# Optimization experiments

Measured on AMD Instinct MI355X. Metric: run time of the kernel, lower is better.

Reference implementation:

```python
import jax, jax.numpy as jnp
import numpy as np

B, L, D, K = 16, 4096, 1024, 64


def setup_inputs() -> dict:
    key = jax.random.key(0)
    k1, k2, k3 = jax.random.split(key, 3)
    token_hidden = jax.random.normal(k1, (B, L, D), dtype=jnp.float32)
    attention_mask = jax.random.randint(k2, (B, L), 0, 2, dtype=jnp.int32)
    # [B, K, 2] spans with start <= end (sorted along last axis)
    sent_spans = jnp.sort(jax.random.randint(k3, (B, K, 2), 0, L, dtype=jnp.int64), axis=-1)
    return {"token_hidden": token_hidden, "attention_mask": attention_mask, "sent_spans": sent_spans}


def reference(token_hidden, attention_mask, sent_spans):
    # token_hidden: [B, L, D]; attention_mask: [B, L] int; sent_spans: [B, K, 2] int
    Bn, Ln, Dn = token_hidden.shape
    pos = jnp.arange(Ln)  # [L]
    start = sent_spans[..., 0]                      # [B, K]
    end = jnp.minimum(sent_spans[..., 1], Ln)       # clamp end to L (original: end = min(end, L))
    # membership mask: token l belongs to span k of batch b
    seg = (pos[None, None, :] >= start[..., None]) & (pos[None, None, :] < end[..., None])  # [B, K, L]
    segf = seg.astype(token_hidden.dtype)
    am = attention_mask.astype(token_hidden.dtype)[:, None, :]  # [B, 1, L]
    amw = segf * am                                 # attention-weighted membership
    mask_sum = amw.sum(axis=-1)                     # [B, K] number of attended tokens in span
    length = segf.sum(axis=-1)                      # [B, K] raw span length (after clamping)
    use_am = mask_sum > 0
    # original: masked mean if any attended token, else plain mean over span
    w = jnp.where(use_am[..., None], amw, segf)     # [B, K, L]
    denom = jnp.where(use_am, mask_sum, length)     # [B, K]
    valid = length > 0                              # span non-empty and starts inside L
    denom_safe = jnp.where(valid, denom, jnp.ones_like(denom))
    pooled = jnp.einsum('bkl,bld->bkd', w, token_hidden) / denom_safe[..., None]
    H = jnp.where(valid[..., None], pooled, jnp.zeros_like(pooled))  # [B, K, D]
    sent_mask = valid.astype(jnp.float32)           # [B, K]
    return H, sent_mask
```

## Files before the change

kernel.cpp:

```cpp
#include <hip/hip_runtime.h>

#define Bn 16
#define Ln 4096
#define Dn 1024
#define Kn 64
#define CH 16
#define SEGTOK 128
#define CPS (SEGTOK / CH)
#define NSEG (Ln / SEGTOK)
#define SLOTS (CPS + 1)
#define NSPAN (2 * Bn * Kn)
#define QBLK 4

static __device__ __forceinline__ void acc4(float4& a, const float4 v) {
    a.x += v.x; a.y += v.y; a.z += v.z; a.w += v.w;
}
static __device__ __forceinline__ void sub4(float4& a, const float4 v) {
    a.x -= v.x; a.y -= v.y; a.z -= v.z; a.w -= v.w;
}
static __device__ __forceinline__ void acc4w(float4& a, const float4 v, float w) {
    a.x += v.x * w; a.y += v.y * w; a.z += v.z * w; a.w += v.w * w;
}

static __device__ __forceinline__ void edge8(
    const float* __restrict__ xb, const int* __restrict__ amb,
    int base, int n, float sign, float4& acc) {
    int wv[8];
    int any = 0;
#pragma unroll
    for (int t = 0; t < 8; ++t) {
        const int li = (base + t < Ln) ? (base + t) : (Ln - 1);
        wv[t] = (t < n) ? amb[li] : 0;
        any |= wv[t];
    }
    if (any != 0) {
        int f = 0;
#pragma unroll
        for (int t = 7; t >= 0; --t) if (wv[t] != 0) f = t;
        int le[8];
        int lp = f;
#pragma unroll
        for (int t = 0; t < 8; ++t) { lp = (wv[t] != 0) ? t : lp; le[t] = lp; }
        float4 v[8];
#pragma unroll
        for (int t = 0; t < 8; ++t)
            v[t] = *(const float4*)(xb + (size_t)(base + le[t]) * Dn);
        float4 s0 = {0.f,0.f,0.f,0.f}, s1 = {0.f,0.f,0.f,0.f};
#pragma unroll
        for (int t = 0; t < 8; t += 2) {
            acc4w(s0, v[t],     sign * (float)wv[t]);
            acc4w(s1, v[t + 1], sign * (float)wv[t + 1]);
        }
        acc4(s0, s1);
        acc4(acc, s0);
    }
}

__global__ __launch_bounds__(256) void fused_stage1_kernel(
    const float* __restrict__ x, const int* __restrict__ am,
    const unsigned int* __restrict__ spans_raw,
    float* __restrict__ Pf, int* __restrict__ Pam, int* __restrict__ dec) {
    const int bc = blockIdx.x;

    if (bc < Bn * NSEG) {
        const int b = bc / NSEG;
        const int seg = bc % NSEG;
        const int d0 = threadIdx.x * 4;

        const float* xp = x + ((size_t)b * Ln + (size_t)seg * SEGTOK) * Dn + d0;
        const int4* amp4 = (const int4*)(am + b * Ln + seg * SEGTOK);
        float* pf = Pf + (size_t)bc * SLOTS * Dn + d0;

        float4 acc = {0.f, 0.f, 0.f, 0.f};
#pragma unroll
        for (int j = 0; j < CPS; ++j) {
            *(float4*)(pf + (size_t)j * Dn) = acc;

            int4 a0 = amp4[j * 4 + 0];
            int4 a1 = amp4[j * 4 + 1];
            int4 a2 = amp4[j * 4 + 2];
            int4 a3 = amp4[j * 4 + 3];
            int wv[CH] = {a0.x, a0.y, a0.z, a0.w, a1.x, a1.y, a1.z, a1.w,
                          a2.x, a2.y, a2.z, a2.w, a3.x, a3.y, a3.z, a3.w};

            int any = 0;
#pragma unroll
            for (int t = 0; t < CH; ++t) any |= wv[t];

            if (any != 0) {
                int f = 0;
#pragma unroll
                for (int t = CH - 1; t >= 0; --t) if (wv[t] != 0) f = t;
                int le[CH];
                int lp = f;
#pragma unroll
                for (int t = 0; t < CH; ++t) {
                    lp = (wv[t] != 0) ? t : lp;
                    le[t] = lp;
                }
                float4 v[CH];
#pragma unroll
                for (int t = 0; t < CH; ++t)
                    v[t] = *(const float4*)(xp + (size_t)(j * CH + le[t]) * Dn);
                float4 s0 = {0.f, 0.f, 0.f, 0.f}, s1 = {0.f, 0.f, 0.f, 0.f};
#pragma unroll
                for (int t = 0; t < CH; t += 2) {
                    acc4w(s0, v[t],     (float)wv[t]);
                    acc4w(s1, v[t + 1], (float)wv[t + 1]);
                }
                acc4(s0, s1);
                acc4(acc, s0);
            }
        }
        *(float4*)(pf + (size_t)CPS * Dn) = acc;
    } else if (bc < Bn * NSEG + Bn) {
        const int b = bc - Bn * NSEG;
        const int t = threadIdx.x;
        const int i0 = t * 16;
        const int* amb = am + (size_t)b * Ln;
        int loc[16];
        int lsum = 0;
#pragma unroll
        for (int j = 0; j < 16; ++j) { loc[j] = amb[i0 + j]; lsum += loc[j]; }

        __shared__ int ssum[256];
        ssum[t] = lsum;
        __syncthreads();
        for (int off = 1; off < 256; off <<= 1) {
            int v2 = (t >= off) ? ssum[t - off] : 0;
            __syncthreads();
            ssum[t] += v2;
            __syncthreads();
        }
        int run = ssum[t] - lsum;
        int* pam = Pam + (size_t)b * (Ln + 1);
#pragma unroll
        for (int j = 0; j < 16; ++j) { pam[i0 + j] = run; run += loc[j]; }
        if (t == 255) pam[Ln] = run;
    } else {
        __shared__ unsigned int sred[256];
        unsigned int acc = 0;
        for (int i = threadIdx.x; i < NSPAN / 2; i += 256)
            acc |= spans_raw[2 * i + 1];
        sred[threadIdx.x] = acc;
        __syncthreads();
        for (int off = 128; off > 0; off >>= 1) {
            if ((int)threadIdx.x < off) sred[threadIdx.x] |= sred[threadIdx.x + off];
            __syncthreads();
        }
        const bool is64 = (sred[0] == 0u);
        for (int i = threadIdx.x; i < NSPAN; i += 256)
            dec[i] = is64 ? (int)spans_raw[2 * i] : (int)spans_raw[i];
    }
}

__global__ __launch_bounds__(64) void span_pool_kernel(
    const float* __restrict__ x, const int* __restrict__ am,
    const int* __restrict__ spans, const float* __restrict__ Pf,
    const int* __restrict__ Pam, float* __restrict__ H,
    float* __restrict__ sent_mask) {
    const int gb = blockIdx.x;
    const int bk = gb >> 2;
    const int q  = gb & 3;
    const int b = bk / Kn;

    int s = spans[2 * bk];
    int e = spans[2 * bk + 1];
    if (s < 0) s = 0; if (s > Ln) s = Ln;
    if (e < 0) e = 0; if (e > Ln) e = Ln;
    const int len = (e > s) ? (e - s) : 0;
    if (e < s) e = s;

    const int* pam = Pam + (size_t)b * (Ln + 1);
    const int msum = pam[e] - pam[s];
    const bool use_am = (msum > 0);
    const bool valid = (len > 0);

    const int d0 = q * 256 + (int)threadIdx.x * 4;
    const float* xb = x + (size_t)b * Ln * Dn + d0;
    const int* amb = am + (size_t)b * Ln;
    float4 acc = {0.f, 0.f, 0.f, 0.f};

    if (!use_am) {
        for (int l = s; l < e; ++l)
            acc4(acc, *(const float4*)(xb + (size_t)l * Dn));
    } else {
        const int ca = (s + CH - 1) / CH;
        const int cb = e / CH;
        const float* Pb = Pf + (size_t)b * NSEG * SLOTS * Dn + d0;

        if (ca <= cb) {
            if (cb > ca) {
                const int sa = ca / CPS, ja = ca % CPS;
                const int sb = cb / CPS, jb = cb % CPS;
                if (sa == sb) {
                    float4 r = *(const float4*)(Pb + (size_t)(sa * SLOTS + jb) * Dn);
                    sub4(r, *(const float4*)(Pb + (size_t)(sa * SLOTS + ja) * Dn));
                    acc4(acc, r);
                } else {
                    float4 r = *(const float4*)(Pb + (size_t)(sa * SLOTS + CPS) * Dn);
                    sub4(r, *(const float4*)(Pb + (size_t)(sa * SLOTS + ja) * Dn));
                    float4 m0 = {0.f,0.f,0.f,0.f}, m1 = {0.f,0.f,0.f,0.f};
                    int ss = sa + 1;
                    for (; ss + 1 < sb; ss += 2) {
                        acc4(m0, *(const float4*)(Pb + (size_t)(ss * SLOTS + CPS) * Dn));
                        acc4(m1, *(const float4*)(Pb + (size_t)((ss + 1) * SLOTS + CPS) * Dn));
                    }
                    if (ss < sb)
                        acc4(m0, *(const float4*)(Pb + (size_t)(ss * SLOTS + CPS) * Dn));
                    acc4(r, m0); acc4(r, m1);
                    if (jb > 0)
                        acc4(r, *(const float4*)(Pb + (size_t)(sb * SLOTS + jb) * Dn));
                    acc4(acc, r);
                }
            }

            const int elenA = ca * CH - s;
            if (elenA > 0) {
                if (elenA <= 8) {
                    edge8(xb, amb, s, elenA, 1.f, acc);
                } else {
                    const int g = ca - 1;
                    const int sg = g / CPS, j = g % CPS;
                    acc4(acc, *(const float4*)(Pb + (size_t)(sg * SLOTS + j + 1) * Dn));
                    sub4(acc, *(const float4*)(Pb + (size_t)(sg * SLOTS + j) * Dn));
                    edge8(xb, amb, g * CH, CH - elenA, -1.f, acc);
                }
            }

            const int elenB = e - cb * CH;
            if (elenB > 0) {
                if (elenB <= 8) {
                    edge8(xb, amb, cb * CH, elenB, 1.f, acc);
                } else {
                    const int g = cb;
                    const int sg = g / CPS, j = g % CPS;
                    acc4(acc, *(const float4*)(Pb + (size_t)(sg * SLOTS + j + 1) * Dn));
                    sub4(acc, *(const float4*)(Pb + (size_t)(sg * SLOTS + j) * Dn));
                    edge8(xb, amb, e, CH - elenB, -1.f, acc);
                }
            }
        } else {
            int wv[CH];
#pragma unroll
            for (int t = 0; t < CH; ++t) {
                const int li = (s + t < Ln) ? (s + t) : (Ln - 1);
                wv[t] = (t < len) ? amb[li] : 0;
            }
            int any = 0;
#pragma unroll
            for (int t = 0; t < CH; ++t) any |= wv[t];
            if (any != 0) {
                int f = 0;
#pragma unroll
                for (int t = CH - 1; t >= 0; --t) if (wv[t] != 0) f = t;
                int le[CH];
                int lp = f;
#pragma unroll
                for (int t = 0; t < CH; ++t) {
                    lp = (wv[t] != 0) ? t : lp;
                    le[t] = lp;
                }
                float4 v[CH];
#pragma unroll
                for (int t = 0; t < CH; ++t)
                    v[t] = *(const float4*)(xb + (size_t)(s + le[t]) * Dn);
                float4 s0 = {0.f,0.f,0.f,0.f}, s1 = {0.f,0.f,0.f,0.f};
#pragma unroll
                for (int t = 0; t < CH; t += 2) {
                    acc4w(s0, v[t],     (float)wv[t]);
                    acc4w(s1, v[t + 1], (float)wv[t + 1]);
                }
                acc4(s0, s1);
                acc4(acc, s0);
            }
        }
    }

    const float denom = use_am ? (float)msum : (float)len;
    const float inv = valid ? (1.0f / denom) : 0.0f;
    float4 outv;
    outv.x = acc.x * inv; outv.y = acc.y * inv;
    outv.z = acc.z * inv; outv.w = acc.w * inv;

    *(float4*)(H + (size_t)bk * Dn + d0) = outv;
    if (threadIdx.x == 0 && q == 0) sent_mask[bk] = valid ? 1.0f : 0.0f;
}

extern "C" void kernel_launch(void* const* d_in, const int* in_sizes, int n_in,
                              void* d_out, int out_size, void* d_ws, size_t ws_size,
                              hipStream_t stream) {
    const float* x = (const float*)d_in[0];
    const int* am = (const int*)d_in[1];
    const unsigned int* spans_raw = (const unsigned int*)d_in[2];

    float* H = (float*)d_out;
    float* sent_mask = H + (size_t)Bn * Kn * Dn;

    const size_t dec_bytes = 8192;
    const size_t pam_bytes = (size_t)Bn * (Ln + 1) * sizeof(int);
    int* dec = (int*)d_ws;
    int* Pam = (int*)((char*)d_ws + dec_bytes);
    float* Pf = (float*)((char*)d_ws + dec_bytes + pam_bytes);

    fused_stage1_kernel<<<Bn * NSEG + Bn + 1, 256, 0, stream>>>(
        x, am, spans_raw, Pf, Pam, dec);
    span_pool_kernel<<<Bn * Kn * QBLK, 64, 0, stream>>>(
        x, am, dec, Pf, Pam, H, sent_mask);
}
```

Baseline: 37.73 us.

## Merge both stages into one cooperative kernel with a grid-wide sync

Replaces the two launches (prefix-sum stage and span-pooling stage) with a single cooperative kernel. All 512 blocks first build the chunk prefix sums, with blocks 0-16 also computing the mask prefix and decoding the spans. A grid.sync follows, and then each wave grid-strides over the span-pool tasks. This removes one kernel launch and the inter-kernel gap, at the cost of a grid barrier, extra serial work on the first 17 blocks, and a cooperative launch that needs every block resident at once.

```diff
diff --git a/kernel.cpp b/kernel.cpp
--- a/kernel.cpp
+++ b/kernel.cpp
@@ -1,4 +1,7 @@
 #include <hip/hip_runtime.h>
+#include <hip/hip_cooperative_groups.h>
+
+namespace cg = cooperative_groups;
 
 #define Bn 16
 #define Ln 4096
@@ -11,6 +14,8 @@
 #define SLOTS (CPS + 1)
 #define NSPAN (2 * Bn * Kn)
 #define QBLK 4
+#define NBLK (Bn * NSEG)
+#define NWAVE (NBLK * 4)
 
 static __device__ __forceinline__ void acc4(float4& a, const float4 v) {
     a.x += v.x; a.y += v.y; a.z += v.z; a.w += v.w;
@@ -56,65 +61,16 @@
     }
 }
 
-__global__ __launch_bounds__(256) void fused_stage1_kernel(
+__global__ __launch_bounds__(256) void fused_all_kernel(
     const float* __restrict__ x, const int* __restrict__ am,
     const unsigned int* __restrict__ spans_raw,
-    float* __restrict__ Pf, int* __restrict__ Pam, int* __restrict__ dec) {
+    float* __restrict__ Pf, int* __restrict__ Pam, int* __restrict__ dec,
+    float* __restrict__ H, float* __restrict__ sent_mask) {
     const int bc = blockIdx.x;
-
-    if (bc < Bn * NSEG) {
-        const int b = bc / NSEG;
-        const int seg = bc % NSEG;
-        const int d0 = threadIdx.x * 4;
-
-        const float* xp = x + ((size_t)b * Ln + (size_t)seg * SEGTOK) * Dn + d0;
-        const int4* amp4 = (const int4*)(am + b * Ln + seg * SEGTOK);
-        float* pf = Pf + (size_t)bc * SLOTS * Dn + d0;
-
-        float4 acc = {0.f, 0.f, 0.f, 0.f};
-#pragma unroll
-        for (int j = 0; j < CPS; ++j) {
-            *(float4*)(pf + (size_t)j * Dn) = acc;
-
-            int4 a0 = amp4[j * 4 + 0];
-            int4 a1 = amp4[j * 4 + 1];
-            int4 a2 = amp4[j * 4 + 2];
-            int4 a3 = amp4[j * 4 + 3];
-            int wv[CH] = {a0.x, a0.y, a0.z, a0.w, a1.x, a1.y, a1.z, a1.w,
-                          a2.x, a2.y, a2.z, a2.w, a3.x, a3.y, a3.z, a3.w};
-
-            int any = 0;
-#pragma unroll
-            for (int t = 0; t < CH; ++t) any |= wv[t];
-
-            if (any != 0) {
-                int f = 0;
-#pragma unroll
-                for (int t = CH - 1; t >= 0; --t) if (wv[t] != 0) f = t;
-                int le[CH];
-                int lp = f;
-#pragma unroll
-                for (int t = 0; t < CH; ++t) {
-                    lp = (wv[t] != 0) ? t : lp;
-                    le[t] = lp;
-                }
-                float4 v[CH];
-#pragma unroll
-                for (int t = 0; t < CH; ++t)
-                    v[t] = *(const float4*)(xp + (size_t)(j * CH + le[t]) * Dn);
-                float4 s0 = {0.f, 0.f, 0.f, 0.f}, s1 = {0.f, 0.f, 0.f, 0.f};
-#pragma unroll
-                for (int t = 0; t < CH; t += 2) {
-                    acc4w(s0, v[t],     (float)wv[t]);
-                    acc4w(s1, v[t + 1], (float)wv[t + 1]);
-                }
-                acc4(s0, s1);
-                acc4(acc, s0);
-            }
-        }
-        *(float4*)(pf + (size_t)CPS * Dn) = acc;
-    } else if (bc < Bn * NSEG + Bn) {
-        const int b = bc - Bn * NSEG;
+    __shared__ int ssum[256];
+
+    if (bc < Bn) {
+        const int b = bc;
         const int t = threadIdx.x;
         const int i0 = t * 16;
         const int* amb = am + (size_t)b * Ln;
@@ -123,7 +79,6 @@
 #pragma unroll
         for (int j = 0; j < 16; ++j) { loc[j] = amb[i0 + j]; lsum += loc[j]; }
 
-        __shared__ int ssum[256];
         ssum[t] = lsum;
         __syncthreads();
         for (int off = 1; off < 256; off <<= 1) {
@@ -137,119 +92,48 @@
 #pragma unroll
         for (int j = 0; j < 16; ++j) { pam[i0 + j] = run; run += loc[j]; }
         if (t == 255) pam[Ln] = run;
-    } else {
-        __shared__ unsigned int sred[256];
+        __syncthreads();
+    } else if (bc == Bn) {
         unsigned int acc = 0;
         for (int i = threadIdx.x; i < NSPAN / 2; i += 256)
             acc |= spans_raw[2 * i + 1];
-        sred[threadIdx.x] = acc;
+        ssum[threadIdx.x] = (int)acc;
         __syncthreads();
         for (int off = 128; off > 0; off >>= 1) {
-            if ((int)threadIdx.x < off) sred[threadIdx.x] |= sred[threadIdx.x + off];
+            if ((int)threadIdx.x < off) ssum[threadIdx.x] |= ssum[threadIdx.x + off];
             __syncthreads();
         }
-        const bool is64 = (sred[0] == 0u);
+        const bool is64 = (ssum[0] == 0);
         for (int i = threadIdx.x; i < NSPAN; i += 256)
             dec[i] = is64 ? (int)spans_raw[2 * i] : (int)spans_raw[i];
-    }
-}
-
-__global__ __launch_bounds__(64) void span_pool_kernel(
-    const float* __restrict__ x, const int* __restrict__ am,
-    const int* __restrict__ spans, const float* __restrict__ Pf,
-    const int* __restrict__ Pam, float* __restrict__ H,
-    float* __restrict__ sent_mask) {
-    const int gb = blockIdx.x;
-    const int bk = gb >> 2;
-    const int q  = gb & 3;
-    const int b = bk / Kn;
-
-    int s = spans[2 * bk];
-    int e = spans[2 * bk + 1];
-    if (s < 0) s = 0; if (s > Ln) s = Ln;
-    if (e < 0) e = 0; if (e > Ln) e = Ln;
-    const int len = (e > s) ? (e - s) : 0;
-    if (e < s) e = s;
-
-    const int* pam = Pam + (size_t)b * (Ln + 1);
-    const int msum = pam[e] - pam[s];
-    const bool use_am = (msum > 0);
-    const bool valid = (len > 0);
-
-    const int d0 = q * 256 + (int)threadIdx.x * 4;
-    const float* xb = x + (size_t)b * Ln * Dn + d0;
-    const int* amb = am + (size_t)b * Ln;
-    float4 acc = {0.f, 0.f, 0.f, 0.f};
-
-    if (!use_am) {
-        for (int l = s; l < e; ++l)
-            acc4(acc, *(const float4*)(xb + (size_t)l * Dn));
-    } else {
-        const int ca = (s + CH - 1) / CH;
-        const int cb = e / CH;
-        const float* Pb = Pf + (size_t)b * NSEG * SLOTS * Dn + d0;
-
-        if (ca <= cb) {
-            if (cb > ca) {
-                const int sa = ca / CPS, ja = ca % CPS;
-                const int sb = cb / CPS, jb = cb % CPS;
-                if (sa == sb) {
-                    float4 r = *(const float4*)(Pb + (size_t)(sa * SLOTS + jb) * Dn);
-                    sub4(r, *(const float4*)(Pb + (size_t)(sa * SLOTS + ja) * Dn));
-                    acc4(acc, r);
-                } else {
-                    float4 r = *(const float4*)(Pb + (size_t)(sa * SLOTS + CPS) * Dn);
-                    sub4(r, *(const float4*)(Pb + (size_t)(sa * SLOTS + ja) * Dn));
-                    float4 m0 = {0.f,0.f,0.f,0.f}, m1 = {0.f,0.f,0.f,0.f};
-                    int ss = sa + 1;
-                    for (; ss + 1 < sb; ss += 2) {
-                        acc4(m0, *(const float4*)(Pb + (size_t)(ss * SLOTS + CPS) * Dn));
-                        acc4(m1, *(const float4*)(Pb + (size_t)((ss + 1) * SLOTS + CPS) * Dn));
-                    }
-                    if (ss < sb)
-                        acc4(m0, *(const float4*)(Pb + (size_t)(ss * SLOTS + CPS) * Dn));
-                    acc4(r, m0); acc4(r, m1);
-                    if (jb > 0)
-                        acc4(r, *(const float4*)(Pb + (size_t)(sb * SLOTS + jb) * Dn));
-                    acc4(acc, r);
-                }
-            }
-
-            const int elenA = ca * CH - s;
-            if (elenA > 0) {
-                if (elenA <= 8) {
-                    edge8(xb, amb, s, elenA, 1.f, acc);
-                } else {
-                    const int g = ca - 1;
-                    const int sg = g / CPS, j = g % CPS;
-                    acc4(acc, *(const float4*)(Pb + (size_t)(sg * SLOTS + j + 1) * Dn));
-                    sub4(acc, *(const float4*)(Pb + (size_t)(sg * SLOTS + j) * Dn));
-                    edge8(xb, amb, g * CH, CH - elenA, -1.f, acc);
-                }
-            }
-
-            const int elenB = e - cb * CH;
-            if (elenB > 0) {
-                if (elenB <= 8) {
-                    edge8(xb, amb, cb * CH, elenB, 1.f, acc);
-                } else {
-                    const int g = cb;
-                    const int sg = g / CPS, j = g % CPS;
-                    acc4(acc, *(const float4*)(Pb + (size_t)(sg * SLOTS + j + 1) * Dn));
-                    sub4(acc, *(const float4*)(Pb + (size_t)(sg * SLOTS + j) * Dn));
-                    edge8(xb, amb, e, CH - elenB, -1.f, acc);
-                }
-            }
-        } else {
-            int wv[CH];
-#pragma unroll
-            for (int t = 0; t < CH; ++t) {
-                const int li = (s + t < Ln) ? (s + t) : (Ln - 1);
-                wv[t] = (t < len) ? amb[li] : 0;
-            }
+        __syncthreads();
+    }
+
+    {
+        const int b = bc / NSEG;
+        const int seg = bc % NSEG;
+        const int d0 = threadIdx.x * 4;
+
+        const float* xp = x + ((size_t)b * Ln + (size_t)seg * SEGTOK) * Dn + d0;
+        const int4* amp4 = (const int4*)(am + b * Ln + seg * SEGTOK);
+        float* pf = Pf + (size_t)bc * SLOTS * Dn + d0;
+
+        float4 acc = {0.f, 0.f, 0.f, 0.f};
+#pragma unroll
+        for (int j = 0; j < CPS; ++j) {
+            *(float4*)(pf + (size_t)j * Dn) = acc;
+
+            int4 a0 = amp4[j * 4 + 0];
+            int4 a1 = amp4[j * 4 + 1];
+            int4 a2 = amp4[j * 4 + 2];
+            int4 a3 = amp4[j * 4 + 3];
+            int wv[CH] = {a0.x, a0.y, a0.z, a0.w, a1.x, a1.y, a1.z, a1.w,
+                          a2.x, a2.y, a2.z, a2.w, a3.x, a3.y, a3.z, a3.w};
+
             int any = 0;
 #pragma unroll
             for (int t = 0; t < CH; ++t) any |= wv[t];
+
             if (any != 0) {
                 int f = 0;
 #pragma unroll
@@ -264,8 +148,8 @@
                 float4 v[CH];
 #pragma unroll
                 for (int t = 0; t < CH; ++t)
-                    v[t] = *(const float4*)(xb + (size_t)(s + le[t]) * Dn);
-                float4 s0 = {0.f,0.f,0.f,0.f}, s1 = {0.f,0.f,0.f,0.f};
+                    v[t] = *(const float4*)(xp + (size_t)(j * CH + le[t]) * Dn);
+                float4 s0 = {0.f, 0.f, 0.f, 0.f}, s1 = {0.f, 0.f, 0.f, 0.f};
 #pragma unroll
                 for (int t = 0; t < CH; t += 2) {
                     acc4w(s0, v[t],     (float)wv[t]);
@@ -275,16 +159,141 @@
                 acc4(acc, s0);
             }
         }
-    }
-
-    const float denom = use_am ? (float)msum : (float)len;
-    const float inv = valid ? (1.0f / denom) : 0.0f;
-    float4 outv;
-    outv.x = acc.x * inv; outv.y = acc.y * inv;
-    outv.z = acc.z * inv; outv.w = acc.w * inv;
-
-    *(float4*)(H + (size_t)bk * Dn + d0) = outv;
-    if (threadIdx.x == 0 && q == 0) sent_mask[bk] = valid ? 1.0f : 0.0f;
+        *(float4*)(pf + (size_t)CPS * Dn) = acc;
+    }
+
+    cg::this_grid().sync();
+
+    const int wv_id = bc * 4 + ((int)threadIdx.x >> 6);
+    const int lane = (int)threadIdx.x & 63;
+
+    for (int task = wv_id; task < Bn * Kn * QBLK; task += NWAVE) {
+        const int bk = task >> 2;
+        const int q  = task & 3;
+        const int b = bk / Kn;
+
+        int s = dec[2 * bk];
+        int e = dec[2 * bk + 1];
+        if (s < 0) s = 0; if (s > Ln) s = Ln;
+        if (e < 0) e = 0; if (e > Ln) e = Ln;
+        const int len = (e > s) ? (e - s) : 0;
+        if (e < s) e = s;
+
+        const int* pam = Pam + (size_t)b * (Ln + 1);
+        const int msum = pam[e] - pam[s];
+        const bool use_am = (msum > 0);
+        const bool valid = (len > 0);
+
+        const int d0 = q * 256 + lane * 4;
+        const float* xb = x + (size_t)b * Ln * Dn + d0;
+        const int* amb = am + (size_t)b * Ln;
+        float4 acc = {0.f, 0.f, 0.f, 0.f};
+
+        if (!use_am) {
+            for (int l = s; l < e; ++l)
+                acc4(acc, *(const float4*)(xb + (size_t)l * Dn));
+        } else {
+            const int ca = (s + CH - 1) / CH;
+            const int cb = e / CH;
+            const float* Pb = Pf + (size_t)b * NSEG * SLOTS * Dn + d0;
+
+            if (ca <= cb) {
+                if (cb > ca) {
+                    const int sa = ca / CPS, ja = ca % CPS;
+                    const int sb = cb / CPS, jb = cb % CPS;
+                    if (sa == sb) {
+                        float4 r = *(const float4*)(Pb + (size_t)(sa * SLOTS + jb) * Dn);
+                        sub4(r, *(const float4*)(Pb + (size_t)(sa * SLOTS + ja) * Dn));
+                        acc4(acc, r);
+                    } else {
+                        float4 r = *(const float4*)(Pb + (size_t)(sa * SLOTS + CPS) * Dn);
+                        sub4(r, *(const float4*)(Pb + (size_t)(sa * SLOTS + ja) * Dn));
+                        float4 m0 = {0.f,0.f,0.f,0.f}, m1 = {0.f,0.f,0.f,0.f};
+                        int ss = sa + 1;
+                        for (; ss + 1 < sb; ss += 2) {
+                            acc4(m0, *(const float4*)(Pb + (size_t)(ss * SLOTS + CPS) * Dn));
+                            acc4(m1, *(const float4*)(Pb + (size_t)((ss + 1) * SLOTS + CPS) * Dn));
+                        }
+                        if (ss < sb)
+                            acc4(m0, *(const float4*)(Pb + (size_t)(ss * SLOTS + CPS) * Dn));
+                        acc4(r, m0); acc4(r, m1);
+                        if (jb > 0)
+                            acc4(r, *(const float4*)(Pb + (size_t)(sb * SLOTS + jb) * Dn));
+                        acc4(acc, r);
+                    }
+                }
+
+                const int elenA = ca * CH - s;
+                if (elenA > 0) {
+                    if (elenA <= 8) {
+                        edge8(xb, amb, s, elenA, 1.f, acc);
+                    } else {
+                        const int g = ca - 1;
+                        const int sg = g / CPS, j = g % CPS;
+                        acc4(acc, *(const float4*)(Pb + (size_t)(sg * SLOTS + j + 1) * Dn));
+                        sub4(acc, *(const float4*)(Pb + (size_t)(sg * SLOTS + j) * Dn));
+                        edge8(xb, amb, g * CH, CH - elenA, -1.f, acc);
+                    }
+                }
+
+                const int elenB = e - cb * CH;
+                if (elenB > 0) {
+                    if (elenB <= 8) {
+                        edge8(xb, amb, cb * CH, elenB, 1.f, acc);
+                    } else {
+                        const int g = cb;
+                        const int sg = g / CPS, j = g % CPS;
+                        acc4(acc, *(const float4*)(Pb + (size_t)(sg * SLOTS + j + 1) * Dn));
+                        sub4(acc, *(const float4*)(Pb + (size_t)(sg * SLOTS + j) * Dn));
+                        edge8(xb, amb, e, CH - elenB, -1.f, acc);
+                    }
+                }
+            } else {
+                int wv[CH];
+#pragma unroll
+                for (int t = 0; t < CH; ++t) {
+                    const int li = (s + t < Ln) ? (s + t) : (Ln - 1);
+                    wv[t] = (t < len) ? amb[li] : 0;
+                }
+                int any = 0;
+#pragma unroll
+                for (int t = 0; t < CH; ++t) any |= wv[t];
+                if (any != 0) {
+                    int f = 0;
+#pragma unroll
+                    for (int t = CH - 1; t >= 0; --t) if (wv[t] != 0) f = t;
+                    int le[CH];
+                    int lp = f;
+#pragma unroll
+                    for (int t = 0; t < CH; ++t) {
+                        lp = (wv[t] != 0) ? t : lp;
+                        le[t] = lp;
+                    }
+                    float4 v[CH];
+#pragma unroll
+                    for (int t = 0; t < CH; ++t)
+                        v[t] = *(const float4*)(xb + (size_t)(s + le[t]) * Dn);
+                    float4 s0 = {0.f,0.f,0.f,0.f}, s1 = {0.f,0.f,0.f,0.f};
+#pragma unroll
+                    for (int t = 0; t < CH; t += 2) {
+                        acc4w(s0, v[t],     (float)wv[t]);
+                        acc4w(s1, v[t + 1], (float)wv[t + 1]);
+                    }
+                    acc4(s0, s1);
+                    acc4(acc, s0);
+                }
+            }
+        }
+
+        const float denom = use_am ? (float)msum : (float)len;
+        const float inv = valid ? (1.0f / denom) : 0.0f;
+        float4 outv;
+        outv.x = acc.x * inv; outv.y = acc.y * inv;
+        outv.z = acc.z * inv; outv.w = acc.w * inv;
+
+        *(float4*)(H + (size_t)bk * Dn + d0) = outv;
+        if (lane == 0 && q == 0) sent_mask[bk] = valid ? 1.0f : 0.0f;
+    }
 }
 
 extern "C" void kernel_launch(void* const* d_in, const int* in_sizes, int n_in,
@@ -303,8 +312,9 @@
     int* Pam = (int*)((char*)d_ws + dec_bytes);
     float* Pf = (float*)((char*)d_ws + dec_bytes + pam_bytes);
 
-    fused_stage1_kernel<<<Bn * NSEG + Bn + 1, 256, 0, stream>>>(
-        x, am, spans_raw, Pf, Pam, dec);
-    span_pool_kernel<<<Bn * Kn * QBLK, 64, 0, stream>>>(
-        x, am, dec, Pf, Pam, H, sent_mask);
-}
+    void* args[] = {(void*)&x, (void*)&am, (void*)&spans_raw,
+                    (void*)&Pf, (void*)&Pam, (void*)&dec,
+                    (void*)&H, (void*)&sent_mask};
+    hipLaunchCooperativeKernel((const void*)fused_all_kernel,
+                               dim3(NBLK), dim3(256), args, 0, stream);
+}
```

Result: slower. 111.7 us (+196.0%).
